# Kernel tuning notes

Hardware: AMD Instinct MI355X
Metric: run time of the kernel (lower is better)

## Reference

```python
import jax, jax.numpy as jnp
import numpy as np

N = 100000      # nodes
E = 1600000     # edges (before self-loops)
IN = 128        # in_channels
HID = 32        # hidden_channels
H = 4           # heads of conv1
OUT = 40        # out_channels (classes)
NEG_SLOPE = 0.2 # PyG GATConv default


def _gat_layer(x, edge_index, W, att_src, att_dst, bias, heads, ch, concat):
    """PyG-style GATConv (add_self_loops=True, eval mode so no dropout).
    x: [n, d_in]; W: [d_in, heads*ch]; att_src/att_dst: [heads, ch]; bias: [heads*ch] or [ch]."""
    n = x.shape[0]
    loops = jnp.arange(n, dtype=edge_index.dtype)
    src = jnp.concatenate([edge_index[0], loops])   # [E+n] message sources (x_j)
    dst = jnp.concatenate([edge_index[1], loops])   # [E+n] message targets (x_i)

    h = (x @ W).reshape(n, heads, ch)               # [n, H, C]
    a_s = jnp.sum(h * att_src, axis=-1)             # [n, H] -> alpha_j component
    a_d = jnp.sum(h * att_dst, axis=-1)             # [n, H] -> alpha_i component

    e = jax.nn.leaky_relu(a_s[src] + a_d[dst], NEG_SLOPE)      # [E+n, H]
    # segment softmax over destination node
    m = jax.ops.segment_max(e, dst, num_segments=n)            # [n, H]
    p = jnp.exp(e - m[dst])
    s = jax.ops.segment_sum(p, dst, num_segments=n)            # [n, H]
    alpha = p / (s[dst] + 1e-16)                                # [E+n, H]

    out = jax.ops.segment_sum(h[src] * alpha[:, :, None], dst, num_segments=n)  # [n, H, C]
    out = out.reshape(n, heads * ch) if concat else out.mean(axis=1)
    return out + bias


def setup_inputs() -> dict:
    key = jax.random.key(0)
    ks = jax.random.split(key, 10)
    sc1 = 1.0 / np.sqrt(IN)
    sc2 = 1.0 / np.sqrt(H * HID)
    return {
        "x": jax.random.normal(ks[0], (N, IN), dtype=jnp.float32),
        "edge_index": jax.random.randint(ks[1], (2, E), 0, N, dtype=jnp.int64),
        "W1": jax.random.normal(ks[2], (IN, H * HID), dtype=jnp.float32) * sc1,
        "a_src1": jax.random.normal(ks[3], (H, HID), dtype=jnp.float32) * sc1,
        "a_dst1": jax.random.normal(ks[4], (H, HID), dtype=jnp.float32) * sc1,
        "b1": jnp.zeros((H * HID,), dtype=jnp.float32),
        "W2": jax.random.normal(ks[5], (H * HID, OUT), dtype=jnp.float32) * sc2,
        "a_src2": jax.random.normal(ks[6], (1, OUT), dtype=jnp.float32) * sc2,
        "a_dst2": jax.random.normal(ks[7], (1, OUT), dtype=jnp.float32) * sc2,
        "b2": jnp.zeros((OUT,), dtype=jnp.float32),
    }


def reference(x, edge_index, W1, a_src1, a_dst1, b1, W2, a_src2, a_dst2, b2):
    h = _gat_layer(x, edge_index, W1, a_src1, a_dst1, b1, heads=H, ch=HID, concat=True)
    h = jax.nn.elu(h)
    # dropout is identity in eval mode
    h = _gat_layer(h, edge_index, W2, a_src2, a_dst2, b2, heads=1, ch=OUT, concat=False)
    return jax.nn.log_softmax(h, axis=1)
```

## Files before the change

### kernel.cpp

```cpp
#include <hip/hip_runtime.h>

#define N_NODES 100000
#define N_EDGES 1600000
#define N_ETOT  1700000
#define NB_BUCK   391
#define PART_BLOCKS 512
#define PART_CHUNK  3328

typedef unsigned int uint32;
typedef __attribute__((ext_vector_type(8))) short bf16x8;
typedef __attribute__((ext_vector_type(4))) float f32x4;

__device__ __forceinline__ unsigned short f2bf(float f) {
  uint32 u = __float_as_uint(f);
  u += 0x7FFFu + ((u >> 16) & 1u);
  return (unsigned short)(u >> 16);
}
__device__ __forceinline__ float bf_lo(uint32 w) { return __uint_as_float(w << 16); }
__device__ __forceinline__ float bf_hi(uint32 w) { return __uint_as_float(w & 0xFFFF0000u); }


__global__ __launch_bounds__(256) void k_bcount(const int* __restrict__ ei,
                                                int* __restrict__ bcnt) {
  __shared__ int hist[NB_BUCK];
  const int t = threadIdx.x;
  for (int b = t; b < NB_BUCK; b += 256) hist[b] = 0;
  __syncthreads();
  const int c0 = blockIdx.x * PART_CHUNK;
  const int c1 = (c0 + PART_CHUNK < N_ETOT) ? c0 + PART_CHUNK : N_ETOT;
  for (int i = c0 + t; i < c1; i += 256) {
    int dst = (i < N_EDGES) ? ei[N_EDGES + i] : (i - N_EDGES);
    atomicAdd(&hist[dst >> 8], 1);
  }
  __syncthreads();
  for (int b = t; b < NB_BUCK; b += 256)
    if (hist[b]) atomicAdd(&bcnt[b], hist[b]);
}

__global__ void k_bscan(const int* __restrict__ bcnt, int* __restrict__ pbase,
                        int* __restrict__ bcur, int* __restrict__ rs) {
  __shared__ int sm[512];
  int t = threadIdx.x;
  int v = (t < NB_BUCK) ? bcnt[t] : 0;
  sm[t] = v;
  __syncthreads();
  for (int off = 1; off < 512; off <<= 1) {
    int xv = (t >= off) ? sm[t - off] : 0;
    __syncthreads();
    sm[t] += xv;
    __syncthreads();
  }
  if (t < NB_BUCK) { int e = sm[t] - v; pbase[t] = e; bcur[t] = e; }
  if (t == 0) { pbase[NB_BUCK] = N_ETOT; rs[N_NODES] = N_ETOT; }
}

__global__ __launch_bounds__(256) void k_part(const int* __restrict__ ei,
                                              int* __restrict__ bcur,
                                              uint32* __restrict__ pairs) {
  __shared__ int hist[NB_BUCK];
  __shared__ int base[NB_BUCK];
  const int t = threadIdx.x;
  for (int b = t; b < NB_BUCK; b += 256) hist[b] = 0;
  __syncthreads();
  const int c0 = blockIdx.x * PART_CHUNK;
  const int c1 = (c0 + PART_CHUNK < N_ETOT) ? c0 + PART_CHUNK : N_ETOT;
  for (int i = c0 + t; i < c1; i += 256) {
    int dst = (i < N_EDGES) ? ei[N_EDGES + i] : (i - N_EDGES);
    atomicAdd(&hist[dst >> 8], 1);
  }
  __syncthreads();
  for (int b = t; b < NB_BUCK; b += 256) {
    int h = hist[b];
    base[b] = h ? atomicAdd(&bcur[b], h) : 0;
    hist[b] = 0;
  }
  __syncthreads();
  for (int i = c0 + t; i < c1; i += 256) {
    int src, dst;
    if (i < N_EDGES) { src = ei[i]; dst = ei[N_EDGES + i]; }
    else             { src = i - N_EDGES; dst = src; }
    int b = dst >> 8;
    int r = atomicAdd(&hist[b], 1);
    pairs[base[b] + r] = (uint32)src | (((uint32)dst & 255u) << 17);
  }
}

__global__ __launch_bounds__(256) void k_scatter2f(const int* __restrict__ pbase,
                                                   const uint32* __restrict__ pairs,
                                                   int* __restrict__ rs,
                                                   int* __restrict__ csr) {
  __shared__ int cnt[256];
  __shared__ int scn[256];
  __shared__ int cur[256];
  const int t = threadIdx.x;
  const int lo = blockIdx.x << 8;
  cnt[t] = 0;
  __syncthreads();
  const int p0 = pbase[blockIdx.x], p1 = pbase[blockIdx.x + 1];
  for (int i = p0 + t; i < p1; i += 256) atomicAdd(&cnt[pairs[i] >> 17], 1);
  __syncthreads();
  int v = cnt[t];
  scn[t] = v;
  __syncthreads();
  for (int off = 1; off < 256; off <<= 1) {
    int xv = (t >= off) ? scn[t - off] : 0;
    __syncthreads();
    scn[t] += xv;
    __syncthreads();
  }
  int e = p0 + scn[t] - v;
  cur[t] = e;
  if (lo + t < N_NODES) rs[lo + t] = e;
  __syncthreads();
  for (int i = p0 + t; i < p1; i += 256) {
    uint32 pr = pairs[i];
    int pos = atomicAdd(&cur[pr >> 17], 1);
    csr[pos] = (int)(pr & 0x1FFFFu);
  }
}


__global__ void k_prep(const float* __restrict__ W1, const float* __restrict__ W2,
                       unsigned short* __restrict__ W1t, unsigned short* __restrict__ W2t) {
  int i = blockIdx.x * 256 + threadIdx.x;
  if (i < 128 * 128) {
    int c = i >> 7, k = i & 127;
    W1t[i] = f2bf(W1[k * 128 + c]);
  }
  int j = i - 128 * 128;
  if (j >= 0 && j < 48 * 128) {
    int c = j >> 7, k = j & 127;
    W2t[j] = (c < 40) ? f2bf(W2[k * 40 + c]) : (unsigned short)0;
  }
}


__global__ __launch_bounds__(256) void k_gemm1m(const float* __restrict__ x,
                                                const unsigned short* __restrict__ W1t,
                                                const float* __restrict__ aS1,
                                                const float* __restrict__ aD1,
                                                unsigned short* __restrict__ h1b,
                                                float* __restrict__ s1s,
                                                float* __restrict__ s1d) {
  __shared__ unsigned short As[128 * 128];
  const int t = threadIdx.x;
  const int rbase = blockIdx.x * 128;
  const float4* x4 = (const float4*)x;
  #pragma unroll
  for (int it = 0; it < 8; ++it) {
    int idx = it * 256 + t;
    int r = idx >> 4, c = idx & 15;
    int gr = rbase + r;
    float4 f0 = make_float4(0.f, 0.f, 0.f, 0.f), f1 = f0;
    if (gr < N_NODES) { f0 = x4[(size_t)gr * 32 + c * 2]; f1 = x4[(size_t)gr * 32 + c * 2 + 1]; }
    ushort4 u0, u1;
    u0.x = f2bf(f0.x); u0.y = f2bf(f0.y); u0.z = f2bf(f0.z); u0.w = f2bf(f0.w);
    u1.x = f2bf(f1.x); u1.y = f2bf(f1.y); u1.z = f2bf(f1.z); u1.w = f2bf(f1.w);
    int sc = c ^ (r & 7);
    *(ushort4*)&As[r * 128 + sc * 8] = u0;
    *(ushort4*)&As[r * 128 + sc * 8 + 4] = u1;
  }
  __syncthreads();

  const int wid = t >> 6, lane = t & 63;
  const int wm = wid >> 1, wn = wid & 1;
  const int m0 = wm * 64, n0 = wn * 64;
  const int lr = lane & 15, lk = lane >> 4;

  bf16x8 b[4][4];
  float as_v[4], ad_v[4];
  #pragma unroll
  for (int nt = 0; nt < 4; ++nt) {
    int col = n0 + nt * 16 + lr;
    as_v[nt] = aS1[col]; ad_v[nt] = aD1[col];
    #pragma unroll
    for (int kk = 0; kk < 4; ++kk)
      b[kk][nt] = *(const bf16x8*)&W1t[col * 128 + kk * 32 + lk * 8];
  }

  f32x4 acc[4][4];
  #pragma unroll
  for (int mt = 0; mt < 4; ++mt)
    #pragma unroll
    for (int nt = 0; nt < 4; ++nt) acc[mt][nt] = (f32x4)(0.f);

  #pragma unroll
  for (int mt = 0; mt < 4; ++mt) {
    int row = m0 + mt * 16 + lr;
    #pragma unroll
    for (int kk = 0; kk < 4; ++kk) {
      int c = kk * 4 + lk;
      int sc = c ^ (row & 7);
      bf16x8 a = *(const bf16x8*)&As[row * 128 + sc * 8];
      #pragma unroll
      for (int nt = 0; nt < 4; ++nt)
        acc[mt][nt] = __builtin_amdgcn_mfma_f32_16x16x32_bf16(a, b[kk][nt], acc[mt][nt], 0, 0, 0);
    }
  }

  #pragma unroll
  for (int mt = 0; mt < 4; ++mt)
    #pragma unroll
    for (int nt = 0; nt < 4; ++nt) {
      int col = n0 + nt * 16 + lr;
      #pragma unroll
      for (int r = 0; r < 4; ++r) {
        int gr = rbase + m0 + mt * 16 + lk * 4 + r;
        if (gr < N_NODES) h1b[(size_t)gr * 128 + col] = f2bf(acc[mt][nt][r]);
      }
    }

  const int h0 = wn * 2;
  #pragma unroll
  for (int mt = 0; mt < 4; ++mt)
    #pragma unroll
    for (int r = 0; r < 4; ++r) {
      float sa0 = acc[mt][0][r] * as_v[0] + acc[mt][1][r] * as_v[1];
      float sa1 = acc[mt][2][r] * as_v[2] + acc[mt][3][r] * as_v[3];
      float da0 = acc[mt][0][r] * ad_v[0] + acc[mt][1][r] * ad_v[1];
      float da1 = acc[mt][2][r] * ad_v[2] + acc[mt][3][r] * ad_v[3];
      #pragma unroll
      for (int m = 1; m < 16; m <<= 1) {
        sa0 += __shfl_xor(sa0, m); sa1 += __shfl_xor(sa1, m);
        da0 += __shfl_xor(da0, m); da1 += __shfl_xor(da1, m);
      }
      if (lr == ((mt << 2) | r)) {
        int gr = rbase + m0 + mt * 16 + lk * 4 + r;
        if (gr < N_NODES) {
          s1s[gr * 4 + h0] = sa0; s1s[gr * 4 + h0 + 1] = sa1;
          s1d[gr * 4 + h0] = da0; s1d[gr * 4 + h0 + 1] = da1;
        }
      }
    }
}

__global__ __launch_bounds__(256) void k_gemm2m(const unsigned short* __restrict__ xab,
                                                const unsigned short* __restrict__ W2t,
                                                const float* __restrict__ aS2,
                                                const float* __restrict__ aD2,
                                                unsigned short* __restrict__ h2b,
                                                float* __restrict__ s2d) {
  __shared__ unsigned short As[128 * 128];
  const int t = threadIdx.x;
  const int rbase = blockIdx.x * 128;
  #pragma unroll
  for (int it = 0; it < 8; ++it) {
    int idx = it * 256 + t;
    int r = idx >> 4, c = idx & 15;
    int gr = rbase + r;
    uint4 v = make_uint4(0u, 0u, 0u, 0u);
    if (gr < N_NODES) v = *(const uint4*)&xab[(size_t)gr * 128 + c * 8];
    int sc = c ^ (r & 7);
    *(uint4*)&As[r * 128 + sc * 8] = v;
  }
  __syncthreads();

  const int wid = t >> 6, lane = t & 63;
  const int m0 = wid * 32;
  const int lr = lane & 15, lk = lane >> 4;

  bf16x8 b[4][3];
  float as_v[3], ad_v[3];
  #pragma unroll
  for (int nt = 0; nt < 3; ++nt) {
    int col = nt * 16 + lr;
    as_v[nt] = (col < 40) ? aS2[col] : 0.f;
    ad_v[nt] = (col < 40) ? aD2[col] : 0.f;
    #pragma unroll
    for (int kk = 0; kk < 4; ++kk)
      b[kk][nt] = *(const bf16x8*)&W2t[col * 128 + kk * 32 + lk * 8];
  }

  f32x4 acc[2][3];
  #pragma unroll
  for (int mt = 0; mt < 2; ++mt)
    #pragma unroll
    for (int nt = 0; nt < 3; ++nt) acc[mt][nt] = (f32x4)(0.f);

  #pragma unroll
  for (int mt = 0; mt < 2; ++mt) {
    int row = m0 + mt * 16 + lr;
    #pragma unroll
    for (int kk = 0; kk < 4; ++kk) {
      int c = kk * 4 + lk;
      int sc = c ^ (row & 7);
      bf16x8 a = *(const bf16x8*)&As[row * 128 + sc * 8];
      #pragma unroll
      for (int nt = 0; nt < 3; ++nt)
        acc[mt][nt] = __builtin_amdgcn_mfma_f32_16x16x32_bf16(a, b[kk][nt], acc[mt][nt], 0, 0, 0);
    }
  }

  #pragma unroll
  for (int mt = 0; mt < 2; ++mt)
    #pragma unroll
    for (int nt = 0; nt < 3; ++nt) {
      int col = nt * 16 + lr;
      if (col < 40) {
        #pragma unroll
        for (int r = 0; r < 4; ++r) {
          int gr = rbase + m0 + mt * 16 + lk * 4 + r;
          if (gr < N_NODES) h2b[(size_t)gr * 64 + col] = f2bf(acc[mt][nt][r]);
        }
      }
    }

  #pragma unroll
  for (int mt = 0; mt < 2; ++mt)
    #pragma unroll
    for (int r = 0; r < 4; ++r) {
      float sa = acc[mt][0][r] * as_v[0] + acc[mt][1][r] * as_v[1] + acc[mt][2][r] * as_v[2];
      float da = acc[mt][0][r] * ad_v[0] + acc[mt][1][r] * ad_v[1] + acc[mt][2][r] * ad_v[2];
      #pragma unroll
      for (int m = 1; m < 16; m <<= 1) {
        sa += __shfl_xor(sa, m); da += __shfl_xor(da, m);
      }
      if (lr == ((mt << 2) | r)) {
        int gr = rbase + m0 + mt * 16 + lk * 4 + r;
        if (gr < N_NODES) {
          *(float*)((char*)h2b + (size_t)gr * 128 + 80) = sa;
          s2d[gr] = da;
        }
      }
    }
}


#define ACC8(A, off, u, p) \
  A[(off)+0] += (p)*bf_lo(u.x); A[(off)+1] += (p)*bf_hi(u.x); \
  A[(off)+2] += (p)*bf_lo(u.y); A[(off)+3] += (p)*bf_hi(u.y); \
  A[(off)+4] += (p)*bf_lo(u.z); A[(off)+5] += (p)*bf_hi(u.z); \
  A[(off)+6] += (p)*bf_lo(u.w); A[(off)+7] += (p)*bf_hi(u.w);

__global__ __launch_bounds__(256) void k_gather1(const int* __restrict__ rs,
                                                 const int* __restrict__ csr,
                                                 const unsigned short* __restrict__ h1b,
                                                 const float* __restrict__ asrc,
                                                 const float* __restrict__ adst,
                                                 const float* __restrict__ bias,
                                                 unsigned short* __restrict__ xab) {
  int gid = blockIdx.x * 256 + threadIdx.x;
  int n = gid >> 3;
  if (n >= N_NODES) return;
  int lane = gid & 7;
  int hh = lane >> 1;
  float adn = adst[n * 4 + hh];
  int beg = rs[n], end = rs[n + 1];
  float s = 0.f;
  float A[16];
  #pragma unroll
  for (int j = 0; j < 16; ++j) A[j] = 0.f;
  const uint4* hp = (const uint4*)h1b;
  const size_t lb = (size_t)lane * 2;
  int i = beg;
  for (; i + 2 <= end; i += 2) {
    int s0 = csr[i], s1 = csr[i + 1];
    float w0 = asrc[s0 * 4 + hh];
    float w1 = asrc[s1 * 4 + hh];
    uint4 x0 = hp[(size_t)s0 * 16 + lb];
    uint4 x1 = hp[(size_t)s0 * 16 + lb + 1];
    uint4 y0 = hp[(size_t)s1 * 16 + lb];
    uint4 y1 = hp[(size_t)s1 * 16 + lb + 1];
    float v0 = w0 + adn; v0 = (v0 > 0.f) ? v0 : 0.2f * v0;
    float v1 = w1 + adn; v1 = (v1 > 0.f) ? v1 : 0.2f * v1;
    float p0 = __expf(v0), p1 = __expf(v1);
    s += p0 + p1;
    ACC8(A, 0, x0, p0); ACC8(A, 8, x1, p0);
    ACC8(A, 0, y0, p1); ACC8(A, 8, y1, p1);
  }
  if (i < end) {
    int s0 = csr[i];
    float v0 = asrc[s0 * 4 + hh] + adn; v0 = (v0 > 0.f) ? v0 : 0.2f * v0;
    uint4 x0 = hp[(size_t)s0 * 16 + lb];
    uint4 x1 = hp[(size_t)s0 * 16 + lb + 1];
    float p0 = __expf(v0);
    s += p0;
    ACC8(A, 0, x0, p0); ACC8(A, 8, x1, p0);
  }
  float inv = 1.f / (s + 1e-16f);
  int c = lane * 16;
  unsigned short us[16];
  #pragma unroll
  for (int j = 0; j < 16; ++j) {
    float ov = A[j] * inv + bias[c + j];
    ov = (ov > 0.f) ? ov : __expf(ov) - 1.f;
    us[j] = f2bf(ov);
  }
  uint4 w0, w1;
  w0.x = (uint32)us[0] | ((uint32)us[1] << 16);
  w0.y = (uint32)us[2] | ((uint32)us[3] << 16);
  w0.z = (uint32)us[4] | ((uint32)us[5] << 16);
  w0.w = (uint32)us[6] | ((uint32)us[7] << 16);
  w1.x = (uint32)us[8] | ((uint32)us[9] << 16);
  w1.y = (uint32)us[10] | ((uint32)us[11] << 16);
  w1.z = (uint32)us[12] | ((uint32)us[13] << 16);
  w1.w = (uint32)us[14] | ((uint32)us[15] << 16);
  *(uint4*)&xab[(size_t)n * 128 + c] = w0;
  *(uint4*)&xab[(size_t)n * 128 + c + 8] = w1;
}

__global__ __launch_bounds__(256) void k_gather2(const int* __restrict__ rs,
                                                 const int* __restrict__ csr,
                                                 const unsigned short* __restrict__ h2b,
                                                 const float* __restrict__ adst,
                                                 const float* __restrict__ bias,
                                                 float* __restrict__ out) {
  int gid = blockIdx.x * 256 + threadIdx.x;
  int n = gid >> 3;
  if (n >= N_NODES) return;
  int lane = gid & 7;
  float adn = adst[n];
  int beg = rs[n], end = rs[n + 1];
  float s = 0.f;
  float c0 = 0.f, c1 = 0.f, c2 = 0.f, c3 = 0.f, c4 = 0.f;
  const char* hb = (const char*)h2b;
  int i = beg;
  for (; i + 2 <= end; i += 2) {
    int s0 = csr[i], s1 = csr[i + 1];
    const char* r0 = hb + (size_t)s0 * 128;
    const char* r1 = hb + (size_t)s1 * 128;
    float w0 = *(const float*)(r0 + 80);
    float w1 = *(const float*)(r1 + 80);
    uint2 a0 = *(const uint2*)(r0 + lane * 8);
    uint2 a1 = *(const uint2*)(r1 + lane * 8);
    unsigned short e0 = *(const unsigned short*)(r0 + 64 + lane * 2);
    unsigned short e1 = *(const unsigned short*)(r1 + 64 + lane * 2);
    float v0 = w0 + adn; v0 = (v0 > 0.f) ? v0 : 0.2f * v0;
    float v1 = w1 + adn; v1 = (v1 > 0.f) ? v1 : 0.2f * v1;
    float p0 = __expf(v0), p1 = __expf(v1);
    s += p0 + p1;
    c0 += p0 * bf_lo(a0.x) + p1 * bf_lo(a1.x);
    c1 += p0 * bf_hi(a0.x) + p1 * bf_hi(a1.x);
    c2 += p0 * bf_lo(a0.y) + p1 * bf_lo(a1.y);
    c3 += p0 * bf_hi(a0.y) + p1 * bf_hi(a1.y);
    c4 += p0 * __uint_as_float(((uint32)e0) << 16) + p1 * __uint_as_float(((uint32)e1) << 16);
  }
  if (i < end) {
    int s0 = csr[i];
    const char* r0 = hb + (size_t)s0 * 128;
    float v0 = *(const float*)(r0 + 80) + adn; v0 = (v0 > 0.f) ? v0 : 0.2f * v0;
    uint2 a0 = *(const uint2*)(r0 + lane * 8);
    unsigned short e0 = *(const unsigned short*)(r0 + 64 + lane * 2);
    float p0 = __expf(v0);
    s += p0;
    c0 += p0 * bf_lo(a0.x); c1 += p0 * bf_hi(a0.x);
    c2 += p0 * bf_lo(a0.y); c3 += p0 * bf_hi(a0.y);
    c4 += p0 * __uint_as_float(((uint32)e0) << 16);
  }
  float inv = 1.f / (s + 1e-16f);
  float4 bv = *(const float4*)&bias[lane * 4];
  float b4 = bias[32 + lane];
  float v0 = c0 * inv + bv.x;
  float v1 = c1 * inv + bv.y;
  float v2 = c2 * inv + bv.z;
  float v3 = c3 * inv + bv.w;
  float v4 = c4 * inv + b4;
  float mx = fmaxf(fmaxf(fmaxf(v0, v1), fmaxf(v2, v3)), v4);
  #pragma unroll
  for (int m = 1; m < 8; m <<= 1) mx = fmaxf(mx, __shfl_xor(mx, m, 8));
  float se = __expf(v0 - mx) + __expf(v1 - mx) + __expf(v2 - mx)
           + __expf(v3 - mx) + __expf(v4 - mx);
  #pragma unroll
  for (int m = 1; m < 8; m <<= 1) se += __shfl_xor(se, m, 8);
  float l = __logf(se) + mx;
  float4 o = make_float4(v0 - l, v1 - l, v2 - l, v3 - l);
  *(float4*)&out[(size_t)n * 40 + lane * 4] = o;
  out[(size_t)n * 40 + 32 + lane] = v4 - l;
}


extern "C" void kernel_launch(void* const* d_in, const int* in_sizes, int n_in,
                              void* d_out, int out_size, void* d_ws, size_t ws_size,
                              hipStream_t stream) {
  const float* x   = (const float*)d_in[0];
  const int*   ei  = (const int*)  d_in[1];
  const float* W1  = (const float*)d_in[2];
  const float* aS1 = (const float*)d_in[3];
  const float* aD1 = (const float*)d_in[4];
  const float* b1  = (const float*)d_in[5];
  const float* W2  = (const float*)d_in[6];
  const float* aS2 = (const float*)d_in[7];
  const float* aD2 = (const float*)d_in[8];
  const float* b2  = (const float*)d_in[9];
  float* out = (float*)d_out;
  (void)in_sizes; (void)n_in; (void)out_size; (void)ws_size;

  unsigned short* W1t = (unsigned short*)d_ws;
  unsigned short* W2t = W1t + 128 * 128;
  unsigned short* h1b = W2t + 48 * 128;
  unsigned short* xab = h1b + (size_t)N_NODES * 128;
  unsigned short* h2b = xab + (size_t)N_NODES * 128;
  float* s1s  = (float*)(h2b + (size_t)N_NODES * 64);
  float* s1d  = s1s + (size_t)N_NODES * 4;
  float* s2d  = s1d + (size_t)N_NODES * 4;
  int* rs    = (int*)(s2d + N_NODES);
  int* bcnt  = rs + N_NODES + 1;
  int* pbase = bcnt + NB_BUCK;
  int* bcur  = pbase + NB_BUCK + 1;
  int* csr   = bcur + NB_BUCK;
  uint32* pairs = (uint32*)(csr + N_ETOT);

  hipMemsetAsync(bcnt, 0, NB_BUCK * sizeof(int), stream);
  k_prep     <<<88, 256, 0, stream>>>(W1, W2, W1t, W2t);
  k_bcount   <<<PART_BLOCKS, 256, 0, stream>>>(ei, bcnt);
  k_bscan    <<<1, 512, 0, stream>>>(bcnt, pbase, bcur, rs);
  k_part     <<<PART_BLOCKS, 256, 0, stream>>>(ei, bcur, pairs);
  k_scatter2f<<<NB_BUCK, 256, 0, stream>>>(pbase, pairs, rs, csr);

  k_gemm1m  <<<(N_NODES + 127) / 128, 256, 0, stream>>>(x, W1t, aS1, aD1, h1b, s1s, s1d);
  k_gather1 <<<(N_NODES * 8 + 255) / 256, 256, 0, stream>>>(rs, csr, h1b, s1s, s1d, b1, xab);

  k_gemm2m  <<<(N_NODES + 127) / 128, 256, 0, stream>>>(xab, W2t, aS2, aD2, h2b, s2d);
  k_gather2 <<<(N_NODES * 8 + 255) / 256, 256, 0, stream>>>(rs, csr, h2b, s2d, b2, out);
}
```

Measured before the change: 234.9 us.

## Use fixed-capacity edge buckets and merge independent preprocessing kernels

```diff
diff --git a/kernel.cpp b/kernel.cpp
--- a/kernel.cpp
+++ b/kernel.cpp
@@ -4,8 +4,11 @@
 #define N_EDGES 1600000
 #define N_ETOT  1700000
 #define NB_BUCK   391
+#define SMAX      5120
 #define PART_BLOCKS 512
 #define PART_CHUNK  3328
+#define PREP_BLOCKS 88
+#define GEMM1_BLOCKS 782
 
 typedef unsigned int uint32;
 typedef __attribute__((ext_vector_type(8))) short bf16x8;
@@ -20,10 +23,29 @@
 __device__ __forceinline__ float bf_hi(uint32 w) { return __uint_as_float(w & 0xFFFF0000u); }
 
 
-__global__ __launch_bounds__(256) void k_bcount(const int* __restrict__ ei,
-                                                int* __restrict__ bcnt) {
+__global__ __launch_bounds__(256) void k_partprep(const int* __restrict__ ei,
+                                                  int* __restrict__ bcnt,
+                                                  uint32* __restrict__ pairs,
+                                                  const float* __restrict__ W1,
+                                                  const float* __restrict__ W2,
+                                                  unsigned short* __restrict__ W1t,
+                                                  unsigned short* __restrict__ W2t) {
   __shared__ int hist[NB_BUCK];
+  __shared__ int base[NB_BUCK];
   const int t = threadIdx.x;
+  if (blockIdx.x >= PART_BLOCKS) {
+    int i = (blockIdx.x - PART_BLOCKS) * 256 + t;
+    if (i < 128 * 128) {
+      int c = i >> 7, k = i & 127;
+      W1t[i] = f2bf(W1[k * 128 + c]);
+    }
+    int j = i - 128 * 128;
+    if (j >= 0 && j < 48 * 128) {
+      int c = j >> 7, k = j & 127;
+      W2t[j] = (c < 40) ? f2bf(W2[k * 40 + c]) : (unsigned short)0;
+    }
+    return;
+  }
   for (int b = t; b < NB_BUCK; b += 256) hist[b] = 0;
   __syncthreads();
   const int c0 = blockIdx.x * PART_CHUNK;
@@ -33,45 +55,9 @@
     atomicAdd(&hist[dst >> 8], 1);
   }
   __syncthreads();
-  for (int b = t; b < NB_BUCK; b += 256)
-    if (hist[b]) atomicAdd(&bcnt[b], hist[b]);
-}
-
-__global__ void k_bscan(const int* __restrict__ bcnt, int* __restrict__ pbase,
-                        int* __restrict__ bcur, int* __restrict__ rs) {
-  __shared__ int sm[512];
-  int t = threadIdx.x;
-  int v = (t < NB_BUCK) ? bcnt[t] : 0;
-  sm[t] = v;
-  __syncthreads();
-  for (int off = 1; off < 512; off <<= 1) {
-    int xv = (t >= off) ? sm[t - off] : 0;
-    __syncthreads();
-    sm[t] += xv;
-    __syncthreads();
-  }
-  if (t < NB_BUCK) { int e = sm[t] - v; pbase[t] = e; bcur[t] = e; }
-  if (t == 0) { pbase[NB_BUCK] = N_ETOT; rs[N_NODES] = N_ETOT; }
-}
-
-__global__ __launch_bounds__(256) void k_part(const int* __restrict__ ei,
-                                              int* __restrict__ bcur,
-                                              uint32* __restrict__ pairs) {
-  __shared__ int hist[NB_BUCK];
-  __shared__ int base[NB_BUCK];
-  const int t = threadIdx.x;
-  for (int b = t; b < NB_BUCK; b += 256) hist[b] = 0;
-  __syncthreads();
-  const int c0 = blockIdx.x * PART_CHUNK;
-  const int c1 = (c0 + PART_CHUNK < N_ETOT) ? c0 + PART_CHUNK : N_ETOT;
-  for (int i = c0 + t; i < c1; i += 256) {
-    int dst = (i < N_EDGES) ? ei[N_EDGES + i] : (i - N_EDGES);
-    atomicAdd(&hist[dst >> 8], 1);
-  }
-  __syncthreads();
   for (int b = t; b < NB_BUCK; b += 256) {
     int h = hist[b];
-    base[b] = h ? atomicAdd(&bcur[b], h) : 0;
+    base[b] = h ? (b * SMAX + atomicAdd(&bcnt[b], h)) : 0;
     hist[b] = 0;
   }
   __syncthreads();
@@ -85,66 +71,55 @@
   }
 }
 
-__global__ __launch_bounds__(256) void k_scatter2f(const int* __restrict__ pbase,
+
+__global__ __launch_bounds__(256) void k_scatgemm1(const int* __restrict__ bcnt,
                                                    const uint32* __restrict__ pairs,
-                                                   int* __restrict__ rs,
-                                                   int* __restrict__ csr) {
-  __shared__ int cnt[256];
-  __shared__ int scn[256];
-  __shared__ int cur[256];
-  const int t = threadIdx.x;
-  const int lo = blockIdx.x << 8;
-  cnt[t] = 0;
-  __syncthreads();
-  const int p0 = pbase[blockIdx.x], p1 = pbase[blockIdx.x + 1];
-  for (int i = p0 + t; i < p1; i += 256) atomicAdd(&cnt[pairs[i] >> 17], 1);
-  __syncthreads();
-  int v = cnt[t];
-  scn[t] = v;
-  __syncthreads();
-  for (int off = 1; off < 256; off <<= 1) {
-    int xv = (t >= off) ? scn[t - off] : 0;
-    __syncthreads();
-    scn[t] += xv;
-    __syncthreads();
-  }
-  int e = p0 + scn[t] - v;
-  cur[t] = e;
-  if (lo + t < N_NODES) rs[lo + t] = e;
-  __syncthreads();
-  for (int i = p0 + t; i < p1; i += 256) {
-    uint32 pr = pairs[i];
-    int pos = atomicAdd(&cur[pr >> 17], 1);
-    csr[pos] = (int)(pr & 0x1FFFFu);
-  }
-}
-
-
-__global__ void k_prep(const float* __restrict__ W1, const float* __restrict__ W2,
-                       unsigned short* __restrict__ W1t, unsigned short* __restrict__ W2t) {
-  int i = blockIdx.x * 256 + threadIdx.x;
-  if (i < 128 * 128) {
-    int c = i >> 7, k = i & 127;
-    W1t[i] = f2bf(W1[k * 128 + c]);
-  }
-  int j = i - 128 * 128;
-  if (j >= 0 && j < 48 * 128) {
-    int c = j >> 7, k = j & 127;
-    W2t[j] = (c < 40) ? f2bf(W2[k * 40 + c]) : (unsigned short)0;
-  }
-}
-
-
-__global__ __launch_bounds__(256) void k_gemm1m(const float* __restrict__ x,
-                                                const unsigned short* __restrict__ W1t,
-                                                const float* __restrict__ aS1,
-                                                const float* __restrict__ aD1,
-                                                unsigned short* __restrict__ h1b,
-                                                float* __restrict__ s1s,
-                                                float* __restrict__ s1d) {
+                                                   int2* __restrict__ rse,
+                                                   int* __restrict__ csr,
+                                                   const float* __restrict__ x,
+                                                   const unsigned short* __restrict__ W1t,
+                                                   const float* __restrict__ aS1,
+                                                   const float* __restrict__ aD1,
+                                                   unsigned short* __restrict__ h1b,
+                                                   float* __restrict__ s1s,
+                                                   float* __restrict__ s1d) {
   __shared__ unsigned short As[128 * 128];
   const int t = threadIdx.x;
-  const int rbase = blockIdx.x * 128;
+
+  if (blockIdx.x < NB_BUCK) {
+    int* cnt = (int*)As;
+    int* scn = cnt + 256;
+    int* cur = scn + 256;
+    const int b = blockIdx.x;
+    const int lo = b << 8;
+    cnt[t] = 0;
+    __syncthreads();
+    const int p0 = b * SMAX;
+    const int p1 = p0 + bcnt[b];
+    for (int i = p0 + t; i < p1; i += 256) atomicAdd(&cnt[pairs[i] >> 17], 1);
+    __syncthreads();
+    int v = cnt[t];
+    scn[t] = v;
+    __syncthreads();
+    for (int off = 1; off < 256; off <<= 1) {
+      int xv = (t >= off) ? scn[t - off] : 0;
+      __syncthreads();
+      scn[t] += xv;
+      __syncthreads();
+    }
+    int e = p0 + scn[t] - v;
+    cur[t] = e;
+    if (lo + t < N_NODES) rse[lo + t] = make_int2(e, e + v);
+    __syncthreads();
+    for (int i = p0 + t; i < p1; i += 256) {
+      uint32 pr = pairs[i];
+      int pos = atomicAdd(&cur[pr >> 17], 1);
+      csr[pos] = (int)(pr & 0x1FFFFu);
+    }
+    return;
+  }
+
+  const int rbase = (blockIdx.x - NB_BUCK) * 128;
   const float4* x4 = (const float4*)x;
   #pragma unroll
   for (int it = 0; it < 8; ++it) {
@@ -332,7 +307,7 @@
   A[(off)+4] += (p)*bf_lo(u.z); A[(off)+5] += (p)*bf_hi(u.z); \
   A[(off)+6] += (p)*bf_lo(u.w); A[(off)+7] += (p)*bf_hi(u.w);
 
-__global__ __launch_bounds__(256) void k_gather1(const int* __restrict__ rs,
+__global__ __launch_bounds__(256) void k_gather1(const int2* __restrict__ rse,
                                                  const int* __restrict__ csr,
                                                  const unsigned short* __restrict__ h1b,
                                                  const float* __restrict__ asrc,
@@ -345,7 +320,8 @@
   int lane = gid & 7;
   int hh = lane >> 1;
   float adn = adst[n * 4 + hh];
-  int beg = rs[n], end = rs[n + 1];
+  int2 be = rse[n];
+  int beg = be.x, end = be.y;
   float s = 0.f;
   float A[16];
   #pragma unroll
@@ -399,7 +375,7 @@
   *(uint4*)&xab[(size_t)n * 128 + c + 8] = w1;
 }
 
-__global__ __launch_bounds__(256) void k_gather2(const int* __restrict__ rs,
+__global__ __launch_bounds__(256) void k_gather2(const int2* __restrict__ rse,
                                                  const int* __restrict__ csr,
                                                  const unsigned short* __restrict__ h2b,
                                                  const float* __restrict__ adst,
@@ -410,7 +386,8 @@
   if (n >= N_NODES) return;
   int lane = gid & 7;
   float adn = adst[n];
-  int beg = rs[n], end = rs[n + 1];
+  int2 be = rse[n];
+  int beg = be.x, end = be.y;
   float s = 0.f;
   float c0 = 0.f, c1 = 0.f, c2 = 0.f, c3 = 0.f, c4 = 0.f;
   const char* hb = (const char*)h2b;
@@ -493,23 +470,16 @@
   float* s1s  = (float*)(h2b + (size_t)N_NODES * 64);
   float* s1d  = s1s + (size_t)N_NODES * 4;
   float* s2d  = s1d + (size_t)N_NODES * 4;
-  int* rs    = (int*)(s2d + N_NODES);
-  int* bcnt  = rs + N_NODES + 1;
-  int* pbase = bcnt + NB_BUCK;
-  int* bcur  = pbase + NB_BUCK + 1;
-  int* csr   = bcur + NB_BUCK;
-  uint32* pairs = (uint32*)(csr + N_ETOT);
+  int2* rse  = (int2*)(s2d + N_NODES);
+  int* bcnt  = (int*)(rse + N_NODES);
+  int* csr   = bcnt + NB_BUCK;
+  uint32* pairs = (uint32*)(csr + NB_BUCK * SMAX);
 
   hipMemsetAsync(bcnt, 0, NB_BUCK * sizeof(int), stream);
-  k_prep     <<<88, 256, 0, stream>>>(W1, W2, W1t, W2t);
-  k_bcount   <<<PART_BLOCKS, 256, 0, stream>>>(ei, bcnt);
-  k_bscan    <<<1, 512, 0, stream>>>(bcnt, pbase, bcur, rs);
-  k_part     <<<PART_BLOCKS, 256, 0, stream>>>(ei, bcur, pairs);
-  k_scatter2f<<<NB_BUCK, 256, 0, stream>>>(pbase, pairs, rs, csr);
-
-  k_gemm1m  <<<(N_NODES + 127) / 128, 256, 0, stream>>>(x, W1t, aS1, aD1, h1b, s1s, s1d);
-  k_gather1 <<<(N_NODES * 8 + 255) / 256, 256, 0, stream>>>(rs, csr, h1b, s1s, s1d, b1, xab);
-
-  k_gemm2m  <<<(N_NODES + 127) / 128, 256, 0, stream>>>(xab, W2t, aS2, aD2, h2b, s2d);
-  k_gather2 <<<(N_NODES * 8 + 255) / 256, 256, 0, stream>>>(rs, csr, h2b, s2d, b2, out);
-}
+  k_partprep <<<PART_BLOCKS + PREP_BLOCKS, 256, 0, stream>>>(ei, bcnt, pairs, W1, W2, W1t, W2t);
+  k_scatgemm1<<<NB_BUCK + GEMM1_BLOCKS, 256, 0, stream>>>(bcnt, pairs, rse, csr,
+                                                          x, W1t, aS1, aD1, h1b, s1s, s1d);
+  k_gather1  <<<(N_NODES * 8 + 255) / 256, 256, 0, stream>>>(rse, csr, h1b, s1s, s1d, b1, xab);
+  k_gemm2m   <<<GEMM1_BLOCKS, 256, 0, stream>>>(xab, W2t, aS2, aD2, h2b, s2d);
+  k_gather2  <<<(N_NODES * 8 + 255) / 256, 256, 0, stream>>>(rse, csr, h2b, s2d, b2, out);
+}
```

Result: faster. 206.2 us (-12.2%).
